# Optimization experiments

Hardware: AMD Instinct MI355X
Metric: run time of the kernel (lower is better)

Reference implementation:

```python
import jax, jax.numpy as jnp
import numpy as np
from jax import lax

B_, H_, W_, DM = 4, 56, 56, 96
DI = int(2.0 * DM)          # d_inner = 192
NS = 16                     # d_state
RK = int(np.ceil(DM / 16))  # dt_rank = 6
KG = 4                      # scan directions
EPS = 1e-5


def setup_inputs() -> dict:
    key = jax.random.key(0)
    ks = jax.random.split(key, 10)
    x = jax.random.normal(ks[0], (B_, H_, W_, DM), jnp.float32)
    in_proj_w = jax.random.normal(ks[1], (2 * DI, DM), jnp.float32) * (1.0 / np.sqrt(DM))
    conv_w = jax.random.normal(ks[2], (DI, 1, 3, 3), jnp.float32) * (1.0 / 3.0)
    conv_b = jax.random.normal(ks[3], (DI,), jnp.float32) * 0.02
    x_proj_weight = jax.random.normal(ks[4], (KG, RK + 2 * NS, DI), jnp.float32) * (1.0 / np.sqrt(DI))
    dt_projs_weight = jax.random.normal(ks[5], (KG, DI, RK), jnp.float32) * (1.0 / np.sqrt(RK))
    dt_projs_bias = jax.random.uniform(ks[6], (KG, DI), jnp.float32, -4.0, -2.0)  # softplus -> small dt
    A_logs = jnp.tile(jnp.log(jnp.arange(1, NS + 1, dtype=jnp.float32))[None, :], (KG * DI, 1))
    Ds = jnp.ones((KG * DI,), jnp.float32)
    ln_w = jnp.ones((DI,), jnp.float32)
    ln_b = jnp.zeros((DI,), jnp.float32)
    out_proj_w = jax.random.normal(ks[7], (DM, DI), jnp.float32) * (1.0 / np.sqrt(DI))
    return dict(x=x, in_proj_w=in_proj_w, conv_w=conv_w, conv_b=conv_b,
                x_proj_weight=x_proj_weight, dt_projs_weight=dt_projs_weight,
                dt_projs_bias=dt_projs_bias, A_logs=A_logs, Ds=Ds,
                ln_w=ln_w, ln_b=ln_b, out_proj_w=out_proj_w)


def selective_scan(u, delta, A, Bm, Cm, Dv, delta_bias):
    # u, delta: [B,K,D,L]; A: [K,D,N]; Bm, Cm: [B,K,N,L]; Dv, delta_bias: [K,D]
    delta = jax.nn.softplus(delta + delta_bias[None, :, :, None])
    u_l = jnp.moveaxis(u, -1, 0)      # [L,B,K,D]
    d_l = jnp.moveaxis(delta, -1, 0)  # [L,B,K,D]
    B_l = jnp.moveaxis(Bm, -1, 0)     # [L,B,K,N]
    C_l = jnp.moveaxis(Cm, -1, 0)     # [L,B,K,N]
    N = A.shape[-1]
    h0 = jnp.zeros(u.shape[:3] + (N,), u.dtype)  # [B,K,D,N]

    def step(h, inp):
        u_t, d_t, b_t, c_t = inp
        dA = jnp.exp(d_t[..., None] * A)                       # [B,K,D,N]
        h = dA * h + (d_t * u_t)[..., None] * b_t[:, :, None, :]
        y = jnp.einsum('bkdn,bkn->bkd', h, c_t)
        return h, y

    _, ys = lax.scan(step, h0, (u_l, d_l, B_l, C_l))           # ys: [L,B,K,D]
    return jnp.moveaxis(ys, 0, -1) + u * Dv[None, :, :, None]  # [B,K,D,L]


def forward(x, in_proj_w, conv_w, conv_b, x_proj_weight, dt_projs_weight,
            dt_projs_bias, A_logs, Ds, ln_w, ln_b, out_proj_w):
    B, H, W, _ = x.shape
    Di = conv_w.shape[0]
    L = H * W
    xz = x @ in_proj_w.T                       # [B,H,W,2*Di]
    xx, z = jnp.split(xz, 2, axis=-1)
    z = jax.nn.silu(z)
    xc = jnp.transpose(xx, (0, 3, 1, 2))       # [B,Di,H,W]
    xc = lax.conv_general_dilated(xc, conv_w, (1, 1), ((1, 1), (1, 1)),
                                  feature_group_count=Di,
                                  dimension_numbers=('NCHW', 'OIHW', 'NCHW'))
    xc = jax.nn.silu(xc + conv_b[None, :, None, None])
    # cross-scan: identity, transpose(HW), and their flips
    x_flat = xc.reshape(B, Di, L)
    x_wh = jnp.transpose(xc, (0, 1, 3, 2)).reshape(B, Di, L)
    x_hwwh = jnp.stack([x_flat, x_wh], axis=1)                       # [B,2,Di,L]
    xs = jnp.concatenate([x_hwwh, jnp.flip(x_hwwh, axis=-1)], axis=1)  # [B,4,Di,L]
    x_dbl = jnp.einsum('bkdl,kcd->bkcl', xs, x_proj_weight)
    R = dt_projs_weight.shape[-1]
    N = A_logs.shape[-1]
    dts, Bs, Cs = jnp.split(x_dbl, [R, R + N], axis=2)               # [B,K,R,L],[B,K,N,L],[B,K,N,L]
    dts = jnp.einsum('bkrl,kdr->bkdl', dts, dt_projs_weight)         # [B,K,Di,L]
    A = -jnp.exp(A_logs).reshape(KG, Di, N)
    Dv = Ds.reshape(KG, Di)
    out_y = selective_scan(xs, dts, A, Bs, Cs, Dv, dt_projs_bias)    # [B,4,Di,L]
    # cross-merge
    inv_y = jnp.flip(out_y[:, 2:4], axis=-1)
    wh_y = jnp.transpose(out_y[:, 1].reshape(B, Di, W, H), (0, 1, 3, 2)).reshape(B, Di, L)
    invwh_y = jnp.transpose(inv_y[:, 1].reshape(B, Di, W, H), (0, 1, 3, 2)).reshape(B, Di, L)
    y = out_y[:, 0] + inv_y[:, 0] + wh_y + invwh_y                   # [B,Di,L]
    y = jnp.transpose(y, (0, 2, 1))                                  # [B,L,Di]
    mu = y.mean(-1, keepdims=True)
    var = ((y - mu) ** 2).mean(-1, keepdims=True)
    y = (y - mu) / jnp.sqrt(var + EPS) * ln_w + ln_b
    y = y.reshape(B, H, W, Di) * z
    return y @ out_proj_w.T                                          # [B,H,W,d_model]


def reference(x, in_proj_w, conv_w, conv_b, x_proj_weight, dt_projs_weight,
              dt_projs_bias, A_logs, Ds, ln_w, ln_b, out_proj_w):
    return forward(x, in_proj_w, conv_w, conv_b, x_proj_weight, dt_projs_weight,
                   dt_projs_bias, A_logs, Ds, ln_w, ln_b, out_proj_w)
```

## Files before the change

### kernel.cpp

```cpp
#include <hip/hip_runtime.h>
#include <hip/hip_bf16.h>
#include <math.h>

#define BB 4
#define HH 56
#define WW 56
#define DM 96
#define DI 192
#define NS 16
#define RK 6
#define KG 4
#define LL (HH*WW)
#define NPIX (BB*LL)
#define CHL 32
#define NCH (LL/CHL)
#define NDT (DI/16)
#define XP 32
#define NC 38
#define PAD 196
#define LNPX 8

static __device__ __forceinline__ int qmap(int k, int l){
    int m = (k & 2) ? (LL - 1 - l) : l;
    if (k & 1) { int w = m / HH; int h = m % HH; return h * WW + w; }
    return m;
}

static __device__ __forceinline__ float silu(float x){ return x / (1.f + __expf(-x)); }

__global__ __launch_bounds__(256) void k_prep(const float* __restrict__ Win,
    const float* __restrict__ Wout, const float* __restrict__ dtw,
    float* __restrict__ WinT, float* __restrict__ WoutT, float* __restrict__ dtwT)
{
    int t = blockIdx.x*256 + threadIdx.x;
    if (t < 384*DM){
        int i = t / 384, c = t % 384;
        WinT[t] = Win[(size_t)c*DM + i];
    } else if (t < 384*DM + DI*DM){
        int t2 = t - 384*DM;
        int i = t2 / DM, c = t2 % DM;
        WoutT[t2] = Wout[(size_t)c*DI + i];
    } else if (t < 384*DM + DI*DM + KG*RK*DI){
        int t2 = t - 384*DM - DI*DM;
        int k = t2 / (RK*DI);
        int r = (t2 % (RK*DI)) / DI;
        int d = t2 % DI;
        dtwT[t2] = dtw[((size_t)k*DI + d)*RK + r];
    }
}

__global__ __launch_bounds__(384) void k_inproj(const float* __restrict__ x,
        const float* __restrict__ WinT,
        float* __restrict__ conv_in, float* __restrict__ z_silu)
{
    __shared__ float sx[8*DM];
    int pb  = blockIdx.x * 8;
    int c = threadIdx.x;
    sx[c]       = x[(size_t)pb*DM + c];
    sx[c + 384] = x[(size_t)pb*DM + 384 + c];
    __syncthreads();
    float a0=0,a1=0,a2=0,a3=0,a4=0,a5=0,a6=0,a7=0;
    #pragma unroll 4
    for (int i = 0; i < DM; ++i){
        float w = WinT[(size_t)i*384 + c];
        a0=fmaf(sx[i],w,a0);        a1=fmaf(sx[DM+i],w,a1);
        a2=fmaf(sx[2*DM+i],w,a2);   a3=fmaf(sx[3*DM+i],w,a3);
        a4=fmaf(sx[4*DM+i],w,a4);   a5=fmaf(sx[5*DM+i],w,a5);
        a6=fmaf(sx[6*DM+i],w,a6);   a7=fmaf(sx[7*DM+i],w,a7);
    }
    if (c < DI){
        conv_in[(size_t)(pb+0)*DI+c]=a0; conv_in[(size_t)(pb+1)*DI+c]=a1;
        conv_in[(size_t)(pb+2)*DI+c]=a2; conv_in[(size_t)(pb+3)*DI+c]=a3;
        conv_in[(size_t)(pb+4)*DI+c]=a4; conv_in[(size_t)(pb+5)*DI+c]=a5;
        conv_in[(size_t)(pb+6)*DI+c]=a6; conv_in[(size_t)(pb+7)*DI+c]=a7;
    } else {
        int d = c - DI;
        z_silu[(size_t)(pb+0)*DI+d]=silu(a0); z_silu[(size_t)(pb+1)*DI+d]=silu(a1);
        z_silu[(size_t)(pb+2)*DI+d]=silu(a2); z_silu[(size_t)(pb+3)*DI+d]=silu(a3);
        z_silu[(size_t)(pb+4)*DI+d]=silu(a4); z_silu[(size_t)(pb+5)*DI+d]=silu(a5);
        z_silu[(size_t)(pb+6)*DI+d]=silu(a6); z_silu[(size_t)(pb+7)*DI+d]=silu(a7);
    }
}

__global__ __launch_bounds__(256) void k_conv(const float* __restrict__ conv_in,
    const float* __restrict__ cw, const float* __restrict__ cb,
    float* __restrict__ xc)
{
    __shared__ float scw[DI*9];
    int tid = threadIdx.x;
    for (int t = tid; t < DI*9; t += 256) scw[t] = cw[t];
    __syncthreads();
    int idx = blockIdx.x*256 + tid;
    int d = idx % DI;
    int p = (idx / DI) % LL;
    int b = idx / (DI*LL);
    int h = p / WW, w = p % WW;
    float acc = cb[d];
    #pragma unroll
    for (int dy = -1; dy <= 1; ++dy){
        int hy = h + dy; if (hy < 0 || hy >= HH) continue;
        #pragma unroll
        for (int dx = -1; dx <= 1; ++dx){
            int wx = w + dx; if (wx < 0 || wx >= WW) continue;
            acc = fmaf(conv_in[((size_t)b*LL + hy*WW + wx)*DI + d],
                       scw[d*9 + (dy+1)*3 + (dx+1)], acc);
        }
    }
    xc[idx] = silu(acc);
}

static __device__ __forceinline__ float dot4(float4 u, float4 w, float acc){
    acc = fmaf(u.x,w.x,acc); acc = fmaf(u.y,w.y,acc);
    acc = fmaf(u.z,w.z,acc); acc = fmaf(u.w,w.w,acc);
    return acc;
}

static __device__ __forceinline__ float mkdelta(const float* tr, const float* w,
                                                float bb){
    float a = bb;
    #pragma unroll
    for (int r = 0; r < RK; ++r) a = fmaf(tr[r], w[r], a);
    return (a > 20.f) ? a : __logf(1.f + __expf(a));
}

#define HSP(i, pw, comp) h[i] = fmaf(pw, h[i], dlu*(comp))
#define YS(i, comp) y = fmaf(h[i], (comp), y)

__global__ __launch_bounds__(320, 6) void k_xproj(const float* __restrict__ xc,
   const float* __restrict__ xpw, const float* __restrict__ dtb,
   const float* __restrict__ dtwT,
   float* __restrict__ dts, float* __restrict__ Bsb, float* __restrict__ Csb,
   float* __restrict__ hend, float* __restrict__ sumdl)
{
    __shared__ float su[XP*PAD];
    __shared__ float sxd[XP][40];
    int gb = blockIdx.x;
    int bk = gb / NCH, ch = gb % NCH;
    int b = bk >> 2, k = bk & 3;
    int l0 = ch*XP;
    int tid = threadIdx.x;

    for (int t = tid; t < XP*48; t += 320){
        int lo = t / 48, i4 = t % 48;
        int px = qmap(k, l0 + lo);
        float4 u = ((const float4*)(xc + ((size_t)b*LL + px)*DI))[i4];
        *((float4*)&su[lo*PAD + i4*4]) = u;
    }
    __syncthreads();

    if (tid < 19*16){
        int q = tid;
        int c2 = q >> 4, lo = q & 15;
        int c0 = 2*c2, c1 = c0 + 1;
        const float4* p0 = (const float4*)(xpw + ((size_t)k*NC + c0)*DI);
        const float4* p1 = (const float4*)(xpw + ((size_t)k*NC + c1)*DI);
        const float4* ua = (const float4*)&su[lo*PAD];
        const float4* ub = (const float4*)&su[(lo+16)*PAD];
        float a00=0,a01=0,a10=0,a11=0;
        #pragma unroll 4
        for (int i4 = 0; i4 < 48; ++i4){
            float4 u0 = ua[i4], u1 = ub[i4];
            float4 w0 = p0[i4], w1 = p1[i4];
            a00 = dot4(u0,w0,a00); a01 = dot4(u0,w1,a01);
            a10 = dot4(u1,w0,a10); a11 = dot4(u1,w1,a11);
        }
        sxd[lo][c0] = a00;    sxd[lo][c1] = a01;
        sxd[lo+16][c0] = a10; sxd[lo+16][c1] = a11;
    }
    __syncthreads();

    for (int t = tid; t < XP*NS; t += 320){
        int lo = t / NS, n = t % NS;
        Bsb[((size_t)bk*LL + l0+lo)*NS + n] = sxd[lo][RK + n];
        Csb[((size_t)bk*LL + l0+lo)*NS + n] = sxd[lo][RK + NS + n];
    }
    for (int t = tid; t < XP*RK; t += 320){
        int lo = t / RK, r = t % RK;
        dts[((size_t)bk*LL + l0+lo)*RK + r] = sxd[lo][r];
    }

    if (tid < DI){
        int d = tid;
        float wdt[RK];
        {
            const float* wp = dtwT + (size_t)k*RK*DI + d;
            #pragma unroll
            for (int r = 0; r < RK; ++r) wdt[r] = wp[(size_t)r*DI];
        }
        float bb = dtb[k*DI + d];
        float h[NS];
        #pragma unroll
        for (int n = 0; n < NS; ++n) h[n] = 0.f;
        float S = 0.f;
        #pragma unroll 1
        for (int lo = 0; lo < XP; ++lo){
            float uu = su[lo*PAD + d];
            float dl = mkdelta(&sxd[lo][0], wdt, bb);
            S += dl;
            float dlu = dl * uu;
            float r   = __expf(-dl);
            float r2  = r*r,   r3  = r2*r,  r4  = r2*r2;
            float r5  = r4*r,  r6  = r4*r2, r7  = r4*r3,  r8  = r4*r4;
            float r9  = r8*r,  r10 = r8*r2, r11 = r8*r3,  r12 = r8*r4;
            float r13 = r8*r5, r14 = r8*r6, r15 = r8*r7,  r16 = r8*r8;
            const float* bv = &sxd[lo][RK];
            HSP(0, r,  bv[0]);  HSP(1, r2,  bv[1]);  HSP(2, r3,  bv[2]);  HSP(3, r4,  bv[3]);
            HSP(4, r5, bv[4]);  HSP(5, r6,  bv[5]);  HSP(6, r7,  bv[6]);  HSP(7, r8,  bv[7]);
            HSP(8, r9, bv[8]);  HSP(9, r10, bv[9]);  HSP(10, r11, bv[10]); HSP(11, r12, bv[11]);
            HSP(12, r13, bv[12]); HSP(13, r14, bv[13]); HSP(14, r15, bv[14]); HSP(15, r16, bv[15]);
        }
        size_t hb = ((size_t)bk*NCH + ch)*NS*DI + d;
        #pragma unroll
        for (int n = 0; n < NS; ++n) hend[hb + (size_t)n*DI] = h[n];
        sumdl[((size_t)bk*NCH + ch)*DI + d] = S;
    }
}

__global__ __launch_bounds__(256) void k_scan2(float* __restrict__ hend,
    const float* __restrict__ sumdl, const float* __restrict__ Alog)
{
    int blk = blockIdx.x;
    int bk = blk / NDT, part = blk % NDT;
    int k = bk & 3;
    int tid = threadIdx.x;
    int dsub = tid & 15, n = tid >> 4;
    int d = part*16 + dsub;
    float An = -__expf(Alog[((size_t)k*DI + d)*NS + n]);
    size_t base  = ((size_t)bk*NCH)*NS*DI + (size_t)n*DI + d;
    size_t sbase = (size_t)bk*NCH*DI + d;
    float H = 0.f;
    float he0 = hend[base], S0 = sumdl[sbase];
    float he1 = hend[base + (size_t)NS*DI], S1 = sumdl[sbase + DI];
    for (int c = 0; c < NCH; ++c){
        float heN = 0.f, SN = 0.f;
        if (c+2 < NCH){
            heN = hend [base  + (size_t)(c+2)*NS*DI];
            SN  = sumdl[sbase + (size_t)(c+2)*DI];
        }
        hend[base + (size_t)c*NS*DI] = H;
        H  = fmaf(__expf(An*S0), H, he0);
        he0 = he1; S0 = S1;
        he1 = heN; S1 = SN;
    }
}

__global__ __launch_bounds__(192, 6) void k_scan3(const float* __restrict__ dts,
    const float* __restrict__ xc, const float* __restrict__ Bsb,
    const float* __restrict__ Csb,
    const float* __restrict__ dtb, const float* __restrict__ dtwT,
    const float* __restrict__ Dsv, const float* __restrict__ H0,
    float* __restrict__ ys)
{
    __shared__ float sB[CHL][NS], sC[CHL][NS];
    __shared__ float sT[CHL][RK];
    int bid = blockIdx.x;
    int bk = bid / NCH, ch = bid % NCH;
    int b = bk >> 2, k = bk & 3;
    int d = threadIdx.x;
    int l0 = ch*CHL;

    const float* xbase = xc + (size_t)b*LL*DI + d;
    const float* Bb = Bsb + ((size_t)bk*LL + l0)*NS;
    const float* Cb = Csb + ((size_t)bk*LL + l0)*NS;
    const float* Tb = dts + ((size_t)bk*LL + l0)*RK;
    float* ybase = ys + (size_t)bk*LL*DI + d;
    for (int t = d; t < CHL*NS; t += 192){
        ((float*)sB)[t] = Bb[t];
        ((float*)sC)[t] = Cb[t];
    }
    for (int t = d; t < CHL*RK; t += 192) ((float*)sT)[t] = Tb[t];

    float wdt[RK];
    {
        const float* wp = dtwT + (size_t)k*RK*DI + d;
        #pragma unroll
        for (int r = 0; r < RK; ++r) wdt[r] = wp[(size_t)r*DI];
    }
    float bb = dtb[k*DI + d];
    float Dv = Dsv[k*DI + d];

    float h[NS];
    size_t hb = ((size_t)bk*NCH + ch)*NS*DI + d;
    #pragma unroll
    for (int n = 0; n < NS; ++n) h[n] = H0[hb + (size_t)n*DI];
    __syncthreads();

    float pu[2][4];
    int   pq[2][4];
    #pragma unroll
    for (int j = 0; j < 4; ++j){
        pq[0][j] = qmap(k, l0+j);
        pu[0][j] = xbase[(size_t)pq[0][j]*DI];
    }
    #pragma unroll 1
    for (int g = 0; g < CHL/4; ++g){
        int cur = g & 1, nxt = cur ^ 1;
        if (g + 1 < CHL/4){
            #pragma unroll
            for (int j = 0; j < 4; ++j){
                pq[nxt][j] = qmap(k, l0+(g+1)*4+j);
                pu[nxt][j] = xbase[(size_t)pq[nxt][j]*DI];
            }
        }
        #pragma unroll
        for (int j = 0; j < 4; ++j){
            int l = g*4 + j;
            float uu = pu[cur][j];
            float dl = mkdelta(&sT[l][0], wdt, bb);
            float dlu = dl * uu;
            float r   = __expf(-dl);
            float r2  = r*r,   r3  = r2*r,  r4  = r2*r2;
            float r5  = r4*r,  r6  = r4*r2, r7  = r4*r3,  r8  = r4*r4;
            float r9  = r8*r,  r10 = r8*r2, r11 = r8*r3,  r12 = r8*r4;
            float r13 = r8*r5, r14 = r8*r6, r15 = r8*r7,  r16 = r8*r8;
            const float4* br = (const float4*)&sB[l][0];
            const float4* cr = (const float4*)&sC[l][0];
            float4 b0 = br[0], b1 = br[1], b2 = br[2], b3 = br[3];
            HSP(0, r,  b0.x);  HSP(1, r2,  b0.y);  HSP(2, r3,  b0.z);  HSP(3, r4,  b0.w);
            HSP(4, r5, b1.x);  HSP(5, r6,  b1.y);  HSP(6, r7,  b1.z);  HSP(7, r8,  b1.w);
            HSP(8, r9, b2.x);  HSP(9, r10, b2.y);  HSP(10, r11, b2.z); HSP(11, r12, b2.w);
            HSP(12, r13, b3.x); HSP(13, r14, b3.y); HSP(14, r15, b3.z); HSP(15, r16, b3.w);
            float4 c0 = cr[0], c1 = cr[1], c2 = cr[2], c3 = cr[3];
            float y = uu * Dv;
            YS(0,c0.x);  YS(1,c0.y);  YS(2,c0.z);  YS(3,c0.w);
            YS(4,c1.x);  YS(5,c1.y);  YS(6,c1.z);  YS(7,c1.w);
            YS(8,c2.x);  YS(9,c2.y);  YS(10,c2.z); YS(11,c2.w);
            YS(12,c3.x); YS(13,c3.y); YS(14,c3.z); YS(15,c3.w);
            ybase[(size_t)pq[cur][j]*DI] = y;
        }
    }
}

__global__ __launch_bounds__(192) void k_lnout(const float* __restrict__ ys,
    const float* __restrict__ z_silu, const float* __restrict__ lnw,
    const float* __restrict__ lnb, const float* __restrict__ WoutT,
    float* __restrict__ out)
{
    __shared__ float syz[LNPX][DI];
    __shared__ float red_s[LNPX][3], red_q[LNPX][3];
    __shared__ float smu[LNPX], srs[LNPX];
    int pg0 = blockIdx.x * LNPX;
    int b = pg0 / LL, q0 = pg0 % LL;
    int tid = threadIdx.x;
    float wln = lnw[tid], bln = lnb[tid];
    float v[LNPX];
    #pragma unroll
    for (int px = 0; px < LNPX; ++px){
        size_t q = q0 + px;
        const float* r0 = ys + (((size_t)(b*4+0)*LL) + q)*DI + tid;
        const float* r1 = ys + (((size_t)(b*4+1)*LL) + q)*DI + tid;
        const float* r2 = ys + (((size_t)(b*4+2)*LL) + q)*DI + tid;
        const float* r3 = ys + (((size_t)(b*4+3)*LL) + q)*DI + tid;
        v[px] = (*r0 + *r1) + (*r2 + *r3);
    }
    int wid = tid >> 6, lane = tid & 63;
    #pragma unroll
    for (int px = 0; px < LNPX; ++px){
        float s = v[px], sq = v[px]*v[px];
        #pragma unroll
        for (int m = 32; m >= 1; m >>= 1){ s += __shfl_xor(s,m); sq += __shfl_xor(sq,m); }
        if (lane == 0){ red_s[px][wid] = s; red_q[px][wid] = sq; }
    }
    __syncthreads();
    if (tid < LNPX){
        float ts = red_s[tid][0]+red_s[tid][1]+red_s[tid][2];
        float tq = red_q[tid][0]+red_q[tid][1]+red_q[tid][2];
        float mu = ts*(1.f/DI);
        float var = tq*(1.f/DI) - mu*mu;
        smu[tid] = mu; srs[tid] = rsqrtf(var + 1e-5f);
    }
    __syncthreads();
    #pragma unroll
    for (int px = 0; px < LNPX; ++px){
        float z = z_silu[(size_t)(pg0+px)*DI + tid];
        syz[px][tid] = ((v[px]-smu[px])*srs[px]*wln + bln) * z;
    }
    __syncthreads();
    int g = tid / DM, c = tid % DM;
    float a0=0,a1=0,a2=0,a3=0;
    #pragma unroll 4
    for (int i = 0; i < DI; ++i){
        float w = WoutT[(size_t)i*DM + c];
        a0 = fmaf(syz[g*4+0][i], w, a0);
        a1 = fmaf(syz[g*4+1][i], w, a1);
        a2 = fmaf(syz[g*4+2][i], w, a2);
        a3 = fmaf(syz[g*4+3][i], w, a3);
    }
    out[(size_t)(pg0+g*4+0)*DM + c] = a0;
    out[(size_t)(pg0+g*4+1)*DM + c] = a1;
    out[(size_t)(pg0+g*4+2)*DM + c] = a2;
    out[(size_t)(pg0+g*4+3)*DM + c] = a3;
}

extern "C" void kernel_launch(void* const* d_in, const int* in_sizes, int n_in,
                              void* d_out, int out_size, void* d_ws, size_t ws_size,
                              hipStream_t stream)
{
    const float* x    = (const float*)d_in[0];
    const float* Win  = (const float*)d_in[1];
    const float* cw   = (const float*)d_in[2];
    const float* cb   = (const float*)d_in[3];
    const float* xpw  = (const float*)d_in[4];
    const float* dtw  = (const float*)d_in[5];
    const float* dtb  = (const float*)d_in[6];
    const float* Alog = (const float*)d_in[7];
    const float* Dsv  = (const float*)d_in[8];
    const float* lnw  = (const float*)d_in[9];
    const float* lnb  = (const float*)d_in[10];
    const float* Wout = (const float*)d_in[11];
    float* out = (float*)d_out;

    float* ws      = (float*)d_ws;
    float* conv_in = ws;
    float* z_silu  = conv_in + (size_t)NPIX*DI;
    float* xc      = z_silu  + (size_t)NPIX*DI;
    float* ys      = xc      + (size_t)NPIX*DI;
    float* Bsb     = ys      + (size_t)BB*KG*LL*DI;
    float* Csb     = Bsb     + (size_t)BB*KG*LL*NS;
    float* sumdl   = Csb     + (size_t)BB*KG*LL*NS;
    float* dts     = sumdl   + (size_t)BB*KG*NCH*DI;
    float* WinT    = dts     + (size_t)BB*KG*LL*RK;
    float* WoutT   = WinT    + (size_t)DM*2*DI;
    float* dtwT    = WoutT   + (size_t)DI*DM;
    float* hend    = dtwT    + (size_t)KG*RK*DI;

    hipLaunchKernelGGL(k_prep,   dim3((384*DM + DI*DM + KG*RK*DI + 255)/256), dim3(256), 0, stream,
                       Win, Wout, dtw, WinT, WoutT, dtwT);
    hipLaunchKernelGGL(k_inproj, dim3(NPIX/8), dim3(384), 0, stream, x, WinT, conv_in, z_silu);
    hipLaunchKernelGGL(k_conv,   dim3((NPIX*DI)/256), dim3(256), 0, stream, conv_in, cw, cb, xc);
    hipLaunchKernelGGL(k_xproj,  dim3(BB*KG*NCH), dim3(320), 0, stream, xc, xpw, dtb, dtwT,
                       dts, Bsb, Csb, hend, sumdl);
    hipLaunchKernelGGL(k_scan2, dim3(BB*KG*NDT), dim3(256), 0, stream,
                       hend, sumdl, Alog);
    hipLaunchKernelGGL(k_scan3, dim3(BB*KG*NCH), dim3(192), 0, stream,
                       dts, xc, Bsb, Csb, dtb, dtwT, Dsv, hend, ys);
    hipLaunchKernelGGL(k_lnout,  dim3(NPIX/LNPX), dim3(192), 0, stream, ys, z_silu, lnw, lnb, WoutT, out);
}
```

Baseline: 274.6 us.

## Split xproj local scan over two thread halves, deepen scan2 prefetch, store ys as bf16

The chunk-local state scan in k_xproj now uses all 384 threads, with each half handling 8 of the 16 states; the upper half scales its decay powers by r^8. k_scan2 prefetches four chunks ahead instead of two, using a rotating register buffer. The per-direction scan outputs ys are stored as bf16 instead of fp32, halving their write and read traffic between k_scan3 and k_lnout at the cost of reduced precision in the summed outputs before layernorm.

```diff
diff --git a/kernel.cpp b/kernel.cpp
--- a/kernel.cpp
+++ b/kernel.cpp
@@ -126,7 +126,7 @@
 #define HSP(i, pw, comp) h[i] = fmaf(pw, h[i], dlu*(comp))
 #define YS(i, comp) y = fmaf(h[i], (comp), y)
 
-__global__ __launch_bounds__(320, 6) void k_xproj(const float* __restrict__ xc,
+__global__ __launch_bounds__(384, 6) void k_xproj(const float* __restrict__ xc,
    const float* __restrict__ xpw, const float* __restrict__ dtb,
    const float* __restrict__ dtwT,
    float* __restrict__ dts, float* __restrict__ Bsb, float* __restrict__ Csb,
@@ -140,7 +140,7 @@
     int l0 = ch*XP;
     int tid = threadIdx.x;
 
-    for (int t = tid; t < XP*48; t += 320){
+    for (int t = tid; t < XP*48; t += 384){
         int lo = t / 48, i4 = t % 48;
         int px = qmap(k, l0 + lo);
         float4 u = ((const float4*)(xc + ((size_t)b*LL + px)*DI))[i4];
@@ -169,18 +169,19 @@
     }
     __syncthreads();
 
-    for (int t = tid; t < XP*NS; t += 320){
+    for (int t = tid; t < XP*NS; t += 384){
         int lo = t / NS, n = t % NS;
         Bsb[((size_t)bk*LL + l0+lo)*NS + n] = sxd[lo][RK + n];
         Csb[((size_t)bk*LL + l0+lo)*NS + n] = sxd[lo][RK + NS + n];
     }
-    for (int t = tid; t < XP*RK; t += 320){
+    for (int t = tid; t < XP*RK; t += 384){
         int lo = t / RK, r = t % RK;
         dts[((size_t)bk*LL + l0+lo)*RK + r] = sxd[lo][r];
     }
 
-    if (tid < DI){
-        int d = tid;
+    {
+        int o = tid / DI;
+        int d = tid % DI;
         float wdt[RK];
         {
             const float* wp = dtwT + (size_t)k*RK*DI + d;
@@ -188,9 +189,9 @@
             for (int r = 0; r < RK; ++r) wdt[r] = wp[(size_t)r*DI];
         }
         float bb = dtb[k*DI + d];
-        float h[NS];
-        #pragma unroll
-        for (int n = 0; n < NS; ++n) h[n] = 0.f;
+        float h[8];
+        #pragma unroll
+        for (int j = 0; j < 8; ++j) h[j] = 0.f;
         float S = 0.f;
         #pragma unroll 1
         for (int lo = 0; lo < XP; ++lo){
@@ -198,21 +199,20 @@
             float dl = mkdelta(&sxd[lo][0], wdt, bb);
             S += dl;
             float dlu = dl * uu;
-            float r   = __expf(-dl);
-            float r2  = r*r,   r3  = r2*r,  r4  = r2*r2;
-            float r5  = r4*r,  r6  = r4*r2, r7  = r4*r3,  r8  = r4*r4;
-            float r9  = r8*r,  r10 = r8*r2, r11 = r8*r3,  r12 = r8*r4;
-            float r13 = r8*r5, r14 = r8*r6, r15 = r8*r7,  r16 = r8*r8;
-            const float* bv = &sxd[lo][RK];
-            HSP(0, r,  bv[0]);  HSP(1, r2,  bv[1]);  HSP(2, r3,  bv[2]);  HSP(3, r4,  bv[3]);
-            HSP(4, r5, bv[4]);  HSP(5, r6,  bv[5]);  HSP(6, r7,  bv[6]);  HSP(7, r8,  bv[7]);
-            HSP(8, r9, bv[8]);  HSP(9, r10, bv[9]);  HSP(10, r11, bv[10]); HSP(11, r12, bv[11]);
-            HSP(12, r13, bv[12]); HSP(13, r14, bv[13]); HSP(14, r15, bv[14]); HSP(15, r16, bv[15]);
-        }
-        size_t hb = ((size_t)bk*NCH + ch)*NS*DI + d;
-        #pragma unroll
-        for (int n = 0; n < NS; ++n) hend[hb + (size_t)n*DI] = h[n];
-        sumdl[((size_t)bk*NCH + ch)*DI + d] = S;
+            float r  = __expf(-dl);
+            float r2 = r*r,  r3 = r2*r,  r4 = r2*r2;
+            float r5 = r4*r, r6 = r4*r2, r7 = r4*r3, r8 = r4*r4;
+            float m  = o ? r8 : 1.f;
+            const float* bv = &sxd[lo][RK + o*8];
+            HSP(0, r *m, bv[0]); HSP(1, r2*m, bv[1]);
+            HSP(2, r3*m, bv[2]); HSP(3, r4*m, bv[3]);
+            HSP(4, r5*m, bv[4]); HSP(5, r6*m, bv[5]);
+            HSP(6, r7*m, bv[6]); HSP(7, r8*m, bv[7]);
+        }
+        size_t hb = ((size_t)bk*NCH + ch)*NS*DI + (size_t)o*8*DI + d;
+        #pragma unroll
+        for (int j = 0; j < 8; ++j) hend[hb + (size_t)j*DI] = h[j];
+        if (o == 0) sumdl[((size_t)bk*NCH + ch)*DI + d] = S;
     }
 }
 
@@ -229,18 +229,22 @@
     size_t base  = ((size_t)bk*NCH)*NS*DI + (size_t)n*DI + d;
     size_t sbase = (size_t)bk*NCH*DI + d;
     float H = 0.f;
-    float he0 = hend[base], S0 = sumdl[sbase];
-    float he1 = hend[base + (size_t)NS*DI], S1 = sumdl[sbase + DI];
+    float heq[4], Sq[4];
+    #pragma unroll
+    for (int j = 0; j < 4; ++j){
+        heq[j] = hend [base  + (size_t)j*NS*DI];
+        Sq[j]  = sumdl[sbase + (size_t)j*DI];
+    }
     for (int c = 0; c < NCH; ++c){
         float heN = 0.f, SN = 0.f;
-        if (c+2 < NCH){
-            heN = hend [base  + (size_t)(c+2)*NS*DI];
-            SN  = sumdl[sbase + (size_t)(c+2)*DI];
-        }
+        if (c+4 < NCH){
+            heN = hend [base  + (size_t)(c+4)*NS*DI];
+            SN  = sumdl[sbase + (size_t)(c+4)*DI];
+        }
+        int s = c & 3;
         hend[base + (size_t)c*NS*DI] = H;
-        H  = fmaf(__expf(An*S0), H, he0);
-        he0 = he1; S0 = S1;
-        he1 = heN; S1 = SN;
+        H  = fmaf(__expf(An*Sq[s]), H, heq[s]);
+        heq[s] = heN; Sq[s] = SN;
     }
 }
 
@@ -249,7 +253,7 @@
     const float* __restrict__ Csb,
     const float* __restrict__ dtb, const float* __restrict__ dtwT,
     const float* __restrict__ Dsv, const float* __restrict__ H0,
-    float* __restrict__ ys)
+    __hip_bfloat16* __restrict__ ys)
 {
     __shared__ float sB[CHL][NS], sC[CHL][NS];
     __shared__ float sT[CHL][RK];
@@ -263,7 +267,7 @@
     const float* Bb = Bsb + ((size_t)bk*LL + l0)*NS;
     const float* Cb = Csb + ((size_t)bk*LL + l0)*NS;
     const float* Tb = dts + ((size_t)bk*LL + l0)*RK;
-    float* ybase = ys + (size_t)bk*LL*DI + d;
+    __hip_bfloat16* ybase = ys + (size_t)bk*LL*DI + d;
     for (int t = d; t < CHL*NS; t += 192){
         ((float*)sB)[t] = Bb[t];
         ((float*)sC)[t] = Cb[t];
@@ -326,12 +330,12 @@
             YS(4,c1.x);  YS(5,c1.y);  YS(6,c1.z);  YS(7,c1.w);
             YS(8,c2.x);  YS(9,c2.y);  YS(10,c2.z); YS(11,c2.w);
             YS(12,c3.x); YS(13,c3.y); YS(14,c3.z); YS(15,c3.w);
-            ybase[(size_t)pq[cur][j]*DI] = y;
-        }
-    }
-}
-
-__global__ __launch_bounds__(192) void k_lnout(const float* __restrict__ ys,
+            ybase[(size_t)pq[cur][j]*DI] = __float2bfloat16(y);
+        }
+    }
+}
+
+__global__ __launch_bounds__(192) void k_lnout(const __hip_bfloat16* __restrict__ ys,
     const float* __restrict__ z_silu, const float* __restrict__ lnw,
     const float* __restrict__ lnb, const float* __restrict__ WoutT,
     float* __restrict__ out)
@@ -347,11 +351,11 @@
     #pragma unroll
     for (int px = 0; px < LNPX; ++px){
         size_t q = q0 + px;
-        const float* r0 = ys + (((size_t)(b*4+0)*LL) + q)*DI + tid;
-        const float* r1 = ys + (((size_t)(b*4+1)*LL) + q)*DI + tid;
-        const float* r2 = ys + (((size_t)(b*4+2)*LL) + q)*DI + tid;
-        const float* r3 = ys + (((size_t)(b*4+3)*LL) + q)*DI + tid;
-        v[px] = (*r0 + *r1) + (*r2 + *r3);
+        float v0 = __bfloat162float(ys[(((size_t)(b*4+0)*LL) + q)*DI + tid]);
+        float v1 = __bfloat162float(ys[(((size_t)(b*4+1)*LL) + q)*DI + tid]);
+        float v2 = __bfloat162float(ys[(((size_t)(b*4+2)*LL) + q)*DI + tid]);
+        float v3 = __bfloat162float(ys[(((size_t)(b*4+3)*LL) + q)*DI + tid]);
+        v[px] = (v0 + v1) + (v2 + v3);
     }
     int wid = tid >> 6, lane = tid & 63;
     #pragma unroll
@@ -414,8 +418,9 @@
     float* conv_in = ws;
     float* z_silu  = conv_in + (size_t)NPIX*DI;
     float* xc      = z_silu  + (size_t)NPIX*DI;
-    float* ys      = xc      + (size_t)NPIX*DI;
-    float* Bsb     = ys      + (size_t)BB*KG*LL*DI;
+    float* ys_f    = xc      + (size_t)NPIX*DI;
+    __hip_bfloat16* ys = (__hip_bfloat16*)ys_f;
+    float* Bsb     = ys_f    + (size_t)BB*KG*LL*DI/2;
     float* Csb     = Bsb     + (size_t)BB*KG*LL*NS;
     float* sumdl   = Csb     + (size_t)BB*KG*LL*NS;
     float* dts     = sumdl   + (size_t)BB*KG*NCH*DI;
@@ -428,7 +433,7 @@
                        Win, Wout, dtw, WinT, WoutT, dtwT);
     hipLaunchKernelGGL(k_inproj, dim3(NPIX/8), dim3(384), 0, stream, x, WinT, conv_in, z_silu);
     hipLaunchKernelGGL(k_conv,   dim3((NPIX*DI)/256), dim3(256), 0, stream, conv_in, cw, cb, xc);
-    hipLaunchKernelGGL(k_xproj,  dim3(BB*KG*NCH), dim3(320), 0, stream, xc, xpw, dtb, dtwT,
+    hipLaunchKernelGGL(k_xproj,  dim3(BB*KG*NCH), dim3(384), 0, stream, xc, xpw, dtb, dtwT,
                        dts, Bsb, Csb, hend, sumdl);
     hipLaunchKernelGGL(k_scan2, dim3(BB*KG*NDT), dim3(256), 0, stream,
                        hend, sumdl, Alog);
```

Result: slower. 287.8 us (+4.8%).
